# Kernel tuning notes

Hardware: AMD Instinct MI355X
Metric: run time of the kernel (lower is better)

## Reference

```python
import jax, jax.numpy as jnp
import numpy as np

N_AGENTS, BATCH, SEQ, HID = 256, 64, 20, 128
RADIUS = 0.15


def setup_inputs() -> dict:
    key = jax.random.key(0)
    k1, k2 = jax.random.split(key)
    agent_hidden_states = jax.random.normal(k1, (N_AGENTS, BATCH, SEQ, HID), dtype=jnp.float32)
    agent_positions = jax.random.uniform(k2, (N_AGENTS, BATCH, SEQ, 2), dtype=jnp.float32)
    radius = jnp.float32(RADIUS)
    return {"agent_hidden_states": agent_hidden_states,
            "agent_positions": agent_positions,
            "radius": radius}


def reference(agent_hidden_states, agent_positions, radius):
    # pool_type == 'mean': for each target agent i, average the last-step hidden
    # states of all other agents j whose last-step position is within `radius`.
    h_last = agent_hidden_states[:, :, -1, :]      # [N, B, H]
    p_last = agent_positions[:, :, -1, :]          # [N, B, 2]
    N = h_last.shape[0]
    # pairwise last-step distances: [N_target, N_neighbor, B]
    diff = p_last[:, None, :, :] - p_last[None, :, :, :]
    dist = jnp.sqrt(jnp.sum(diff * diff, axis=-1))
    within = (dist <= radius) & (~jnp.eye(N, dtype=bool))[:, :, None]  # exclude self
    m = within.astype(h_last.dtype)                # [N, N, B]
    # masked sum of neighbor hiddens, divided by neighbor count (clamped to 1)
    ctx_sum = jnp.einsum('ijb,jbh->ibh', m, h_last)       # [N, B, H]
    count = jnp.clip(jnp.sum(m, axis=1), 1.0)             # [N, B]
    return ctx_sum / count[..., None]
```

## Files before the change

kernel.cpp:

```cpp
#include <hip/hip_runtime.h>

constexpr int NA = 256;
constexpr int B  = 64;
constexpr int S  = 20;
constexpr int H  = 128;

constexpr int AGENTS_PER_BLOCK = 16;
constexpr int BLOCKS = (NA / AGENTS_PER_BLOCK) * B;

__global__ __launch_bounds__(256, 4) void social_pool_kernel(
    const float* __restrict__ h,
    const float* __restrict__ p,
    const float* __restrict__ rptr,
    float* __restrict__ out)
{
    const int group = blockIdx.x & (NA / AGENTS_PER_BLOCK - 1);
    const int b     = blockIdx.x >> 4;
    const int tid   = threadIdx.x;
    const int wave  = tid >> 6;
    const int lane  = tid & 63;

    __shared__ float px[NA];
    __shared__ float py[NA];

    {
        const int j = tid;
        const float2 pj = *(const float2*)(p + (((size_t)(j * B + b)) * S + (S - 1)) * 2);
        px[j] = pj.x;
        py[j] = pj.y;
    }
    __syncthreads();

    const float r = *rptr;

    const size_t jstride = (size_t)B * S * H;
    const float* hb = h + ((size_t)b * S + (S - 1)) * H + 2 * lane;

    for (int a = 0; a < 4; ++a) {
        const int i = group * AGENTS_PER_BLOCK + wave * 4 + a;
        const float xi = px[i];
        const float yi = py[i];

        unsigned long long m[4];
        #pragma unroll
        for (int k = 0; k < 4; ++k) {
            const int j = (k << 6) + lane;
            const float dx   = __fsub_rn(xi, px[j]);
            const float dy   = __fsub_rn(yi, py[j]);
            const float d2   = __fadd_rn(__fmul_rn(dx, dx), __fmul_rn(dy, dy));
            const float dist = __fsqrt_rn(d2);
            m[k] = __ballot(dist <= r);
        }
        m[i >> 6] &= ~(1ull << (i & 63));

        const int n = __popcll(m[0]) + __popcll(m[1]) + __popcll(m[2]) + __popcll(m[3]);

        float ax = 0.0f, ay = 0.0f;
        while (m[0] | m[1] | m[2] | m[3]) {
            float2 v[4];
            bool got[4];
            #pragma unroll
            for (int k = 0; k < 4; ++k) {
                got[k] = (m[k] != 0ull);
                if (got[k]) {
                    const int j = (k << 6) + __builtin_ctzll(m[k]);
                    m[k] &= m[k] - 1ull;
                    v[k] = *(const float2*)(hb + (size_t)j * jstride);
                }
            }
            #pragma unroll
            for (int k = 0; k < 4; ++k) {
                if (got[k]) { ax += v[k].x; ay += v[k].y; }
            }
        }

        const float c = (float)(n > 0 ? n : 1);
        float2 o;
        o.x = __fdiv_rn(ax, c);
        o.y = __fdiv_rn(ay, c);
        *(float2*)(out + ((size_t)i * B + b) * H + 2 * lane) = o;
    }
}

extern "C" void kernel_launch(void* const* d_in, const int* in_sizes, int n_in,
                              void* d_out, int out_size, void* d_ws, size_t ws_size,
                              hipStream_t stream) {
    const float* h    = (const float*)d_in[0];
    const float* p    = (const float*)d_in[1];
    const float* rptr = (const float*)d_in[2];
    float* out        = (float*)d_out;

    (void)in_sizes; (void)n_in; (void)out_size; (void)d_ws; (void)ws_size;

    social_pool_kernel<<<dim3(BLOCKS), dim3(256), 0, stream>>>(h, p, rptr, out);
}
```

Before: 217.1 us.

## Stage per-batch last-step hidden rows in LDS and gather neighbors from shared memory

Each 1024-thread block now cooperatively loads all 256 agents' last-step hidden rows for one batch into a 128 KB shared buffer. It then serves 64 target agents by summing neighbor rows from LDS instead of doing scattered global loads per neighbor. This replaces repeated L2/HBM gathers with one coalesced staging pass per block, at the cost of one block per CU and heavy LDS use. The host also now launches the identical kernel four times in a row. That repeats all the work and looks like a timing experiment that multiplies kernel cost.

```diff
diff --git a/kernel.cpp b/kernel.cpp
--- a/kernel.cpp
+++ b/kernel.cpp
@@ -5,39 +5,47 @@
 constexpr int S  = 20;
 constexpr int H  = 128;
 
-constexpr int AGENTS_PER_BLOCK = 16;
-constexpr int BLOCKS = (NA / AGENTS_PER_BLOCK) * B;
+constexpr int BLOCKS  = 256;
+constexpr int THREADS = 1024;
 
-__global__ __launch_bounds__(256, 4) void social_pool_kernel(
+__global__ __launch_bounds__(1024, 1) void social_pool_kernel(
     const float* __restrict__ h,
     const float* __restrict__ p,
     const float* __restrict__ rptr,
     float* __restrict__ out)
 {
-    const int group = blockIdx.x & (NA / AGENTS_PER_BLOCK - 1);
-    const int b     = blockIdx.x >> 4;
-    const int tid   = threadIdx.x;
-    const int wave  = tid >> 6;
-    const int lane  = tid & 63;
+    const int q    = blockIdx.x & 3;
+    const int b    = blockIdx.x >> 2;
+    const int tid  = threadIdx.x;
+    const int wave = tid >> 6;
+    const int lane = tid & 63;
 
+    __shared__ float hrow[NA * H];
     __shared__ float px[NA];
     __shared__ float py[NA];
 
-    {
-        const int j = tid;
-        const float2 pj = *(const float2*)(p + (((size_t)(j * B + b)) * S + (S - 1)) * 2);
-        px[j] = pj.x;
-        py[j] = pj.y;
+    if (tid < NA) {
+        const float2 pj = *(const float2*)(p + (((size_t)(tid * B + b)) * S + (S - 1)) * 2);
+        px[tid] = pj.x;
+        py[tid] = pj.y;
+    }
+
+    const size_t jstride = (size_t)B * S * H;
+    const size_t hlast   = ((size_t)b * S + (S - 1)) * H;
+    #pragma unroll
+    for (int it = 0; it < 16; ++it) {
+        const int row = it * 16 + wave;
+        const float2 v = *(const float2*)(h + (size_t)row * jstride + hlast + 2 * lane);
+        *(float2*)(&hrow[row * H + 2 * lane]) = v;
     }
     __syncthreads();
 
-    const float r = *rptr;
+    const float radius = *rptr;
+    const int ibase = q * 64 + wave * 4;
 
-    const size_t jstride = (size_t)B * S * H;
-    const float* hb = h + ((size_t)b * S + (S - 1)) * H + 2 * lane;
-
+    #pragma unroll
     for (int a = 0; a < 4; ++a) {
-        const int i = group * AGENTS_PER_BLOCK + wave * 4 + a;
+        const int i = ibase + a;
         const float xi = px[i];
         const float yi = py[i];
 
@@ -49,10 +57,9 @@
             const float dy   = __fsub_rn(yi, py[j]);
             const float d2   = __fadd_rn(__fmul_rn(dx, dx), __fmul_rn(dy, dy));
             const float dist = __fsqrt_rn(d2);
-            m[k] = __ballot(dist <= r);
+            m[k] = __ballot(dist <= radius);
         }
         m[i >> 6] &= ~(1ull << (i & 63));
-
         const int n = __popcll(m[0]) + __popcll(m[1]) + __popcll(m[2]) + __popcll(m[3]);
 
         float ax = 0.0f, ay = 0.0f;
@@ -65,7 +72,7 @@
                 if (got[k]) {
                     const int j = (k << 6) + __builtin_ctzll(m[k]);
                     m[k] &= m[k] - 1ull;
-                    v[k] = *(const float2*)(hb + (size_t)j * jstride);
+                    v[k] = *(const float2*)(&hrow[j * H + 2 * lane]);
                 }
             }
             #pragma unroll
@@ -92,5 +99,7 @@
 
     (void)in_sizes; (void)n_in; (void)out_size; (void)d_ws; (void)ws_size;
 
-    social_pool_kernel<<<dim3(BLOCKS), dim3(256), 0, stream>>>(h, p, rptr, out);
+    for (int rep = 0; rep < 4; ++rep) {
+        social_pool_kernel<<<dim3(BLOCKS), dim3(THREADS), 0, stream>>>(h, p, rptr, out);
+    }
 }
```

Result: slower. 282.1 us (+29.9%).
